# Kernel optimization log

Measured on AMD Instinct MI355X. Metric: run time of the kernel, lower is better.

The kernel has to match this reference:

```python
import jax, jax.numpy as jnp
import numpy as np

NUM_SAMPLES = 128
NEAR = 0.1
FAR = 2.0
B = 4
NUM_RAYS = 65536


def setup_inputs() -> dict:
    key = jax.random.key(0)
    k1, k2 = jax.random.split(key)
    rgb = jax.random.uniform(k1, (B, NUM_RAYS, NUM_SAMPLES, 3), dtype=jnp.float32)
    density = jax.random.uniform(k2, (B, NUM_RAYS, NUM_SAMPLES), dtype=jnp.float32)
    return {"rgb": rgb, "density": density}


def reference(rgb, density):
    # t_vals: deterministic linspace (eval mode, no stratified noise)
    t_vals = jnp.linspace(NEAR, FAR, NUM_SAMPLES, dtype=jnp.float32)  # [S]
    t_vals = jnp.broadcast_to(t_vals, (B, NUM_RAYS, NUM_SAMPLES))

    # deltas between consecutive samples; last delta is huge (1e10)
    deltas = t_vals[:, :, 1:] - t_vals[:, :, :-1]
    last_delta = jnp.full((B, NUM_RAYS, 1), 1e10, dtype=jnp.float32)
    deltas = jnp.concatenate([deltas, last_delta], axis=2)  # [B,R,S]

    alpha = 1.0 - jnp.exp(-density * deltas)  # [B,R,S]

    # exclusive cumulative product transmittance
    trans_inner = jnp.cumprod(1.0 - alpha + 1e-10, axis=-1)  # [B,R,S]
    ones = jnp.ones((B, NUM_RAYS, 1), dtype=jnp.float32)
    transmittance = jnp.concatenate([ones, trans_inner], axis=-1)[:, :, :-1]  # [B,R,S]

    weights = alpha * transmittance  # [B,R,S]
    rendered_colors = jnp.sum(weights[..., None] * rgb, axis=-2)  # [B,R,3]
    return rendered_colors
```

## Files before the change

### kernel.cpp

```cpp
#include <hip/hip_runtime.h>


#define NSAMP 128
#define NEAR_T 0.1f
#define FAR_T 2.0f

__global__ __launch_bounds__(256) void VolumetricRayMarcher_kernel(
    const float* __restrict__ rgb,
    const float* __restrict__ density,
    float* __restrict__ out,
    int n_rays) {
    const int lane = threadIdx.x & 63;
    const int wave = threadIdx.x >> 6;
    const int ray  = blockIdx.x * 4 + wave;
    if (ray >= n_rays) return;

    const float DELTA = (FAR_T - NEAR_T) / (float)(NSAMP - 1);

    const float2 dpair = ((const float2*)(density + (size_t)ray * NSAMP))[lane];

    const float delta1 = (lane == 63) ? 1e10f : DELTA;

    const float alpha0 = 1.0f - __expf(-dpair.x * DELTA);
    const float alpha1 = 1.0f - __expf(-dpair.y * delta1);
    const float f0 = 1.0f - alpha0 + 1e-10f;
    const float f1 = 1.0f - alpha1 + 1e-10f;

    float p = f0 * f1;
    #pragma unroll
    for (int off = 1; off < 64; off <<= 1) {
        float other = __shfl_up(p, off, 64);
        if (lane >= off) p *= other;
    }
    float excl = __shfl_up(p, 1, 64);
    if (lane == 0) excl = 1.0f;

    const float w0 = alpha0 * excl;
    const float w1 = alpha1 * excl * f0;

    const float2* rgb2 = (const float2*)(rgb + (size_t)ray * NSAMP * 3);
    const float2 a = rgb2[lane * 3 + 0];
    const float2 b = rgb2[lane * 3 + 1];
    const float2 c = rgb2[lane * 3 + 2];
    float cr = w0 * a.x + w1 * b.y;
    float cg = w0 * a.y + w1 * c.x;
    float cb = w0 * b.x + w1 * c.y;

    #pragma unroll
    for (int off = 32; off > 0; off >>= 1) {
        cr += __shfl_xor(cr, off, 64);
        cg += __shfl_xor(cg, off, 64);
        cb += __shfl_xor(cb, off, 64);
    }

    if (lane == 0) {
        float* o = out + (size_t)ray * 3;
        o[0] = cr;
        o[1] = cg;
        o[2] = cb;
    }
}

extern "C" void kernel_launch(void* const* d_in, const int* in_sizes, int n_in,
                              void* d_out, int out_size, void* d_ws, size_t ws_size,
                              hipStream_t stream) {
    const float* rgb     = (const float*)d_in[0];
    const float* density = (const float*)d_in[1];
    float* out = (float*)d_out;

    const int n_rays = in_sizes[1] / NSAMP;
    const int blocks = (n_rays + 3) / 4;

    hipLaunchKernelGGL(VolumetricRayMarcher_kernel, dim3(blocks), dim3(256), 0, stream,
                       rgb, density, out, n_rays);
}
```

Before: 94.79 us.

## Coalesce rgb loads with 16B vectors, scatter weights via LDS, nontemporal I/O

Each lane now loads rgb as one contiguous float4 plus one float2 rather than three strided float2 loads, so accesses are fully contiguous. A per-sample weight table in LDS lets each lane match its loaded channel values to the right sample weight. Loads and the output store are nontemporal, and the output is written by 12 threads per block for coalescing. The change adds an LDS round trip, a block-wide barrier and some select arithmetic on a kernel that is bandwidth bound.

```diff
diff --git a/kernel.cpp b/kernel.cpp
--- a/kernel.cpp
+++ b/kernel.cpp
@@ -2,35 +2,42 @@
 
 
 #define NSAMP 128
-#define NEAR_T 0.1f
-#define FAR_T 2.0f
+typedef float f32x4 __attribute__((ext_vector_type(4)));
+typedef float f32x2 __attribute__((ext_vector_type(2)));
 
 __global__ __launch_bounds__(256) void VolumetricRayMarcher_kernel(
     const float* __restrict__ rgb,
     const float* __restrict__ density,
     float* __restrict__ out,
     int n_rays) {
+    __shared__ float w_lds[4][NSAMP];
+    __shared__ float o_lds[12];
+
     const int lane = threadIdx.x & 63;
     const int wave = threadIdx.x >> 6;
-    const int ray  = blockIdx.x * 4 + wave;
-    if (ray >= n_rays) return;
+    int ray = blockIdx.x * 4 + wave;
+    const bool valid = (ray < n_rays);
+    if (!valid) ray = n_rays - 1;
 
-    const float DELTA = (FAR_T - NEAR_T) / (float)(NSAMP - 1);
+    const float DELTA = (2.0f - 0.1f) / (float)(NSAMP - 1);
 
-    const float2 dpair = ((const float2*)(density + (size_t)ray * NSAMP))[lane];
+    const f32x2 dpair = __builtin_nontemporal_load(
+        (const f32x2*)(density + (size_t)ray * NSAMP) + lane);
+    const float* rbase = rgb + (size_t)ray * (NSAMP * 3);
+    const f32x4 v4 = __builtin_nontemporal_load((const f32x4*)rbase + lane);
+    const f32x2 v2 = __builtin_nontemporal_load((const f32x2*)rbase + 128 + lane);
 
     const float delta1 = (lane == 63) ? 1e10f : DELTA;
-
-    const float alpha0 = 1.0f - __expf(-dpair.x * DELTA);
-    const float alpha1 = 1.0f - __expf(-dpair.y * delta1);
+    const float alpha0 = 1.0f - __expf(-dpair[0] * DELTA);
+    const float alpha1 = 1.0f - __expf(-dpair[1] * delta1);
     const float f0 = 1.0f - alpha0 + 1e-10f;
     const float f1 = 1.0f - alpha1 + 1e-10f;
 
     float p = f0 * f1;
     #pragma unroll
     for (int off = 1; off < 64; off <<= 1) {
-        float other = __shfl_up(p, off, 64);
-        if (lane >= off) p *= other;
+        float o = __shfl_up(p, off, 64);
+        if (lane >= off) p *= o;
     }
     float excl = __shfl_up(p, 1, 64);
     if (lane == 0) excl = 1.0f;
@@ -38,26 +45,49 @@
     const float w0 = alpha0 * excl;
     const float w1 = alpha1 * excl * f0;
 
-    const float2* rgb2 = (const float2*)(rgb + (size_t)ray * NSAMP * 3);
-    const float2 a = rgb2[lane * 3 + 0];
-    const float2 b = rgb2[lane * 3 + 1];
-    const float2 c = rgb2[lane * 3 + 2];
-    float cr = w0 * a.x + w1 * b.y;
-    float cg = w0 * a.y + w1 * c.x;
-    float cb = w0 * b.x + w1 * c.y;
+    ((f32x2*)w_lds[wave])[lane] = f32x2{w0, w1};
+
+    float acc0 = 0.f, acc1 = 0.f, acc2 = 0.f;
+    #pragma unroll
+    for (int k = 0; k < 4; ++k) {
+        const int f = 4 * lane + k;
+        const int s = f / 3;
+        const int c = f - 3 * s;
+        const float t = w_lds[wave][s] * v4[k];
+        acc0 += (c == 0) ? t : 0.0f;
+        acc1 += (c == 1) ? t : 0.0f;
+        acc2 += (c == 2) ? t : 0.0f;
+    }
+    #pragma unroll
+    for (int k = 0; k < 2; ++k) {
+        const int f = 256 + 2 * lane + k;
+        const int s = f / 3;
+        const int c = f - 3 * s;
+        const float t = w_lds[wave][s] * v2[k];
+        acc0 += (c == 0) ? t : 0.0f;
+        acc1 += (c == 1) ? t : 0.0f;
+        acc2 += (c == 2) ? t : 0.0f;
+    }
 
     #pragma unroll
     for (int off = 32; off > 0; off >>= 1) {
-        cr += __shfl_xor(cr, off, 64);
-        cg += __shfl_xor(cg, off, 64);
-        cb += __shfl_xor(cb, off, 64);
+        acc0 += __shfl_xor(acc0, off, 64);
+        acc1 += __shfl_xor(acc1, off, 64);
+        acc2 += __shfl_xor(acc2, off, 64);
     }
 
     if (lane == 0) {
-        float* o = out + (size_t)ray * 3;
-        o[0] = cr;
-        o[1] = cg;
-        o[2] = cb;
+        o_lds[wave * 3 + 0] = acc0;
+        o_lds[wave * 3 + 1] = acc1;
+        o_lds[wave * 3 + 2] = acc2;
+    }
+    __syncthreads();
+
+    const int t = threadIdx.x;
+    if (t < 12) {
+        const int oray = blockIdx.x * 4 + t / 3;
+        if (oray < n_rays)
+            __builtin_nontemporal_store(o_lds[t], out + (size_t)blockIdx.x * 12 + t);
     }
 }
 
```

Result: slower. 104.0 us (+9.7%).

## Process two rays per wavefront with 128-bit vector loads and 32-lane scans

Applied to the files above, without the earlier changes.

Each wavefront now handles two rays, one per 32-lane half. Each lane loads four samples with float4 loads for both density and rgb instead of float2. The transmittance scan and color reduction shrink to 32-lane width, with a short serial product inside each lane. This widens memory transactions, cuts shuffle steps per ray and halves the grid size, at the cost of more registers per thread.

```diff
diff --git a/kernel.cpp b/kernel.cpp
--- a/kernel.cpp
+++ b/kernel.cpp
@@ -2,8 +2,7 @@
 
 
 #define NSAMP 128
-#define NEAR_T 0.1f
-#define FAR_T 2.0f
+typedef float f32x4 __attribute__((ext_vector_type(4)));
 
 __global__ __launch_bounds__(256) void VolumetricRayMarcher_kernel(
     const float* __restrict__ rgb,
@@ -11,53 +10,61 @@
     float* __restrict__ out,
     int n_rays) {
     const int lane = threadIdx.x & 63;
+    const int h    = lane >> 5;
+    const int l    = lane & 31;
     const int wave = threadIdx.x >> 6;
-    const int ray  = blockIdx.x * 4 + wave;
+    const int ray  = blockIdx.x * 8 + wave * 2 + h;
     if (ray >= n_rays) return;
 
-    const float DELTA = (FAR_T - NEAR_T) / (float)(NSAMP - 1);
+    const float DELTA = 1.9f / 127.0f;
 
-    const float2 dpair = ((const float2*)(density + (size_t)ray * NSAMP))[lane];
+    const f32x4 d4 = ((const f32x4*)(density + (size_t)ray * NSAMP))[l];
+    const f32x4* rg = (const f32x4*)(rgb + (size_t)ray * (NSAMP * 3)) + (size_t)l * 3;
+    const f32x4 a = rg[0];
+    const f32x4 b = rg[1];
+    const f32x4 c = rg[2];
 
-    const float delta1 = (lane == 63) ? 1e10f : DELTA;
+    const float dl3 = (l == 31) ? 1e10f : DELTA;
+    const float al0 = 1.0f - __expf(-d4.x * DELTA);
+    const float al1 = 1.0f - __expf(-d4.y * DELTA);
+    const float al2 = 1.0f - __expf(-d4.z * DELTA);
+    const float al3 = 1.0f - __expf(-d4.w * dl3);
+    const float f0 = 1.0f - al0 + 1e-10f;
+    const float f1 = 1.0f - al1 + 1e-10f;
+    const float f2 = 1.0f - al2 + 1e-10f;
+    const float f3 = 1.0f - al3 + 1e-10f;
 
-    const float alpha0 = 1.0f - __expf(-dpair.x * DELTA);
-    const float alpha1 = 1.0f - __expf(-dpair.y * delta1);
-    const float f0 = 1.0f - alpha0 + 1e-10f;
-    const float f1 = 1.0f - alpha1 + 1e-10f;
+    float p = (f0 * f1) * (f2 * f3);
+    #pragma unroll
+    for (int off = 1; off < 32; off <<= 1) {
+        float o = __shfl_up(p, off, 32);
+        if (l >= off) p *= o;
+    }
+    float excl = __shfl_up(p, 1, 32);
+    if (l == 0) excl = 1.0f;
 
-    float p = f0 * f1;
-    #pragma unroll
-    for (int off = 1; off < 64; off <<= 1) {
-        float other = __shfl_up(p, off, 64);
-        if (lane >= off) p *= other;
-    }
-    float excl = __shfl_up(p, 1, 64);
-    if (lane == 0) excl = 1.0f;
+    float t = excl;
+    const float w0 = al0 * t; t *= f0;
+    const float w1 = al1 * t; t *= f1;
+    const float w2 = al2 * t; t *= f2;
+    const float w3 = al3 * t;
 
-    const float w0 = alpha0 * excl;
-    const float w1 = alpha1 * excl * f0;
-
-    const float2* rgb2 = (const float2*)(rgb + (size_t)ray * NSAMP * 3);
-    const float2 a = rgb2[lane * 3 + 0];
-    const float2 b = rgb2[lane * 3 + 1];
-    const float2 c = rgb2[lane * 3 + 2];
-    float cr = w0 * a.x + w1 * b.y;
-    float cg = w0 * a.y + w1 * c.x;
-    float cb = w0 * b.x + w1 * c.y;
+    float acc0 = w0 * a.x + w1 * a.w + w2 * b.z + w3 * c.y;
+    float acc1 = w0 * a.y + w1 * b.x + w2 * b.w + w3 * c.z;
+    float acc2 = w0 * a.z + w1 * b.y + w2 * c.x + w3 * c.w;
 
     #pragma unroll
-    for (int off = 32; off > 0; off >>= 1) {
-        cr += __shfl_xor(cr, off, 64);
-        cg += __shfl_xor(cg, off, 64);
-        cb += __shfl_xor(cb, off, 64);
+    for (int off = 16; off > 0; off >>= 1) {
+        acc0 += __shfl_xor(acc0, off, 32);
+        acc1 += __shfl_xor(acc1, off, 32);
+        acc2 += __shfl_xor(acc2, off, 32);
     }
 
-    if (lane == 0) {
+    if (l == 0) {
         float* o = out + (size_t)ray * 3;
-        o[0] = cr;
-        o[1] = cg;
-        o[2] = cb;
+        o[0] = acc0;
+        o[1] = acc1;
+        o[2] = acc2;
     }
 }
 
@@ -69,7 +76,7 @@
     float* out = (float*)d_out;
 
     const int n_rays = in_sizes[1] / NSAMP;
-    const int blocks = (n_rays + 3) / 4;
+    const int blocks = (n_rays + 7) / 8;
 
     hipLaunchKernelGGL(VolumetricRayMarcher_kernel, dim3(blocks), dim3(256), 0, stream,
                        rgb, density, out, n_rays);
```

Result: no change. 95.28 us (+0.5%).
